# Optimization experiments

Hardware: AMD Instinct MI355X
Metric: run time of the kernel (lower is better)

## Reference

```python
import jax, jax.numpy as jnp
import numpy as np

T = 4096        # tokens
HC = 4          # hc_mult
HID = 4096      # hidden_size
MAX_IT = 20     # max_sk_it (nested: MAX_IT*MAX_IT inner iterations)
EPS = 1e-12


def setup_inputs() -> dict:
    key = jax.random.key(0)
    k1, k2, k3, k4 = jax.random.split(key, 4)
    out_dim = 2 * HC + HC * HC  # 24
    x = jax.random.normal(k1, (T, HC, HID), dtype=jnp.float32)
    weight = jax.random.normal(k2, (HC * HID, out_dim), dtype=jnp.float32) * 0.02
    bias = jax.random.normal(k3, (out_dim,), dtype=jnp.float32) * 0.02
    alpha = 1.0 + 0.1 * jax.random.normal(k4, (3,), dtype=jnp.float32)
    return {"x": x, "weight": weight, "bias": bias, "alpha": alpha}


def reference(x, weight, bias, alpha):
    t, hc, hid = x.shape
    xf = x.reshape(t, hc * hid)
    # RMSNorm scale absorbed into weight; only 1/rms applied explicitly
    r_inv = jax.lax.rsqrt(jnp.mean(xf * xf, axis=-1, keepdims=True))  # [t,1]
    h = xf.astype(jnp.float32) @ weight  # [t, 2*hc + hc*hc]
    h_pre = h[:, :hc]
    h_post = h[:, hc:2 * hc]
    h_res = h[:, 2 * hc:]
    h_pre = jax.nn.sigmoid(r_inv * alpha[0] * h_pre + bias[:hc])
    h_post = 2.0 * jax.nn.sigmoid(r_inv * alpha[1] * h_post + bias[hc:2 * hc])
    h_res_exp = jnp.exp((r_inv * alpha[2] * h_res + bias[2 * hc:]).reshape(t, hc, hc))

    # Sinkhorn-Knopp: original runs max_it outer x max_it inner identical updates
    u0 = jnp.ones((t, hc), jnp.float32)
    v0 = jnp.ones((t, hc), jnp.float32)

    def step(carry, _):
        u, v = carry
        uv = jnp.einsum('tij,tj->ti', h_res_exp, v)
        u = 1.0 / (uv + EPS)
        vu = jnp.einsum('tij,ti->tj', h_res_exp, u)
        v = 1.0 / (vu + EPS)
        return (u, v), None

    (u, v), _ = jax.lax.scan(step, (u0, v0), None, length=MAX_IT * MAX_IT)
    h_res_out = u[:, :, None] * h_res_exp * v[:, None, :]  # [t,hc,hc]
    return h_pre, h_post, h_res_out
```

## Files before the change

kernel.cpp:

```cpp
#include <hip/hip_runtime.h>
#include <hip/hip_bf16.h>


#define TROWS 4096
#define KDIM  16384
#define NOUT  24
#define RG    128
#define KC    32
#define KPER  (KDIM / KC)
#define TILEK 64
#define NTILE (KPER / TILEK)
#define XSTR  (RG + 1)

__device__ __forceinline__ float fast_rcp(float x)   { return __builtin_amdgcn_rcpf(x); }
__device__ __forceinline__ float fast_rsqrt(float x) { return __builtin_amdgcn_rsqf(x); }

__global__ __launch_bounds__(256) void gemv_part(const float* __restrict__ x,
                                                 const float* __restrict__ w,
                                                 float* __restrict__ hacc) {
    __shared__ float xT[TILEK * XSTR];
    __shared__ float wt[TILEK * NOUT];

    const int bid  = blockIdx.x;
    const int rb   = bid & 31;
    const int kc   = bid >> 5;
    const int rg0  = rb * RG;
    const int k0   = kc * KPER;

    const int t    = threadIdx.x;
    const int wv   = t >> 6;
    const int lane = t & 63;

    const int srow = t >> 4;
    const int sf4  = t & 15;
    const int kk   = sf4 * 4;

    float accA[NOUT + 1], accB[NOUT + 1];
#pragma unroll
    for (int j = 0; j <= NOUT; ++j) { accA[j] = 0.0f; accB[j] = 0.0f; }

    const float* xg = x + (size_t)rg0 * KDIM + k0;

    float4 px[8];
    float4 pw0, pw1;
    {
#pragma unroll
        for (int s = 0; s < 8; ++s)
            px[s] = *(const float4*)(xg + (size_t)(srow + 16 * s) * KDIM + kk);
        const float4* wg4 = (const float4*)(w + (size_t)k0 * NOUT);
        pw0 = wg4[t];
        pw1 = (t < 128) ? wg4[256 + t] : pw0;
    }

#pragma unroll 1
    for (int tile = 0; tile < NTILE; ++tile) {
        __syncthreads();
#pragma unroll
        for (int s = 0; s < 8; ++s) {
            const int row = srow + 16 * s;
            xT[(kk + 0) * XSTR + row] = px[s].x;
            xT[(kk + 1) * XSTR + row] = px[s].y;
            xT[(kk + 2) * XSTR + row] = px[s].z;
            xT[(kk + 3) * XSTR + row] = px[s].w;
        }
        ((float4*)wt)[t] = pw0;
        if (t < 128) ((float4*)wt)[256 + t] = pw1;
        __syncthreads();

        const int tn = (tile + 1 < NTILE) ? tile + 1 : tile;
        const int ktn = tn * TILEK;
#pragma unroll
        for (int s = 0; s < 8; ++s)
            px[s] = *(const float4*)(xg + (size_t)(srow + 16 * s) * KDIM + ktn + kk);
        {
            const float4* wg4 = (const float4*)(w + (size_t)(k0 + ktn) * NOUT);
            pw0 = wg4[t];
            pw1 = (t < 128) ? wg4[256 + t] : pw0;
        }

        const float* xk = xT + (wv * 16) * XSTR;
        const float* wk = wt + (wv * 16) * NOUT;
#pragma unroll
        for (int u = 0; u < 16; ++u) {
            const float xa = xk[u * XSTR + lane];
            const float xb = xk[u * XSTR + 64 + lane];
            const float4* wr = (const float4*)(wk + u * NOUT);
            float wbuf[24];
            *(float4*)(wbuf +  0) = wr[0];
            *(float4*)(wbuf +  4) = wr[1];
            *(float4*)(wbuf +  8) = wr[2];
            *(float4*)(wbuf + 12) = wr[3];
            *(float4*)(wbuf + 16) = wr[4];
            *(float4*)(wbuf + 20) = wr[5];
            accA[NOUT] = fmaf(xa, xa, accA[NOUT]);
            accB[NOUT] = fmaf(xb, xb, accB[NOUT]);
#pragma unroll
            for (int j = 0; j < NOUT; ++j) {
                accA[j] = fmaf(wbuf[j], xa, accA[j]);
                accB[j] = fmaf(wbuf[j], xb, accB[j]);
            }
        }
    }

#pragma unroll
    for (int j = 0; j <= NOUT; ++j) {
        atomicAdd(hacc + (size_t)j * TROWS + rg0 + lane,      accA[j]);
        atomicAdd(hacc + (size_t)j * TROWS + rg0 + 64 + lane, accB[j]);
    }
}

__global__ __launch_bounds__(64) void sinkhorn_epilogue(const float* __restrict__ hacc,
                                                        const float* __restrict__ bias,
                                                        const float* __restrict__ alpha,
                                                        float* __restrict__ out) {
    const int row = blockIdx.x * 64 + threadIdx.x;

    float h[25];
#pragma unroll
    for (int j = 0; j < 25; ++j) h[j] = hacc[(size_t)j * TROWS + row];

    const float r_inv = fast_rsqrt(h[24] * (1.0f / (float)KDIM));
    const float a0 = alpha[0], a1 = alpha[1], a2 = alpha[2];

#pragma unroll
    for (int i = 0; i < 4; ++i) {
        const float zpre = fmaf(r_inv * a0, h[i], bias[i]);
        out[(size_t)row * 4 + i] = fast_rcp(1.0f + __expf(-zpre));
        const float zpo = fmaf(r_inv * a1, h[4 + i], bias[4 + i]);
        out[(size_t)16384 + (size_t)row * 4 + i] = 2.0f * fast_rcp(1.0f + __expf(-zpo));
    }

    float E[16];
#pragma unroll
    for (int t = 0; t < 16; ++t)
        E[t] = __expf(fmaf(r_inv * a2, h[8 + t], bias[8 + t]));

    float u0 = 1.0f, u1 = 1.0f, u2 = 1.0f, u3 = 1.0f;
    float v0 = 1.0f, v1 = 1.0f, v2 = 1.0f, v3 = 1.0f;

#pragma unroll 1
    for (int it = 0; it < 400; ++it) {
        float s0 = fmaf(E[0],  v0, fmaf(E[1],  v1, fmaf(E[2],  v2, E[3]  * v3)));
        float s1 = fmaf(E[4],  v0, fmaf(E[5],  v1, fmaf(E[6],  v2, E[7]  * v3)));
        float s2 = fmaf(E[8],  v0, fmaf(E[9],  v1, fmaf(E[10], v2, E[11] * v3)));
        float s3 = fmaf(E[12], v0, fmaf(E[13], v1, fmaf(E[14], v2, E[15] * v3)));
        u0 = fast_rcp(s0 + 1e-12f);
        u1 = fast_rcp(s1 + 1e-12f);
        u2 = fast_rcp(s2 + 1e-12f);
        u3 = fast_rcp(s3 + 1e-12f);
        float t0 = fmaf(E[0], u0, fmaf(E[4], u1, fmaf(E[8],  u2, E[12] * u3)));
        float t1 = fmaf(E[1], u0, fmaf(E[5], u1, fmaf(E[9],  u2, E[13] * u3)));
        float t2 = fmaf(E[2], u0, fmaf(E[6], u1, fmaf(E[10], u2, E[14] * u3)));
        float t3 = fmaf(E[3], u0, fmaf(E[7], u1, fmaf(E[11], u2, E[15] * u3)));
        v0 = fast_rcp(t0 + 1e-12f);
        v1 = fast_rcp(t1 + 1e-12f);
        v2 = fast_rcp(t2 + 1e-12f);
        v3 = fast_rcp(t3 + 1e-12f);
    }

    const size_t ob = 32768 + (size_t)row * 16;
    out[ob + 0]  = u0 * E[0]  * v0;
    out[ob + 1]  = u0 * E[1]  * v1;
    out[ob + 2]  = u0 * E[2]  * v2;
    out[ob + 3]  = u0 * E[3]  * v3;
    out[ob + 4]  = u1 * E[4]  * v0;
    out[ob + 5]  = u1 * E[5]  * v1;
    out[ob + 6]  = u1 * E[6]  * v2;
    out[ob + 7]  = u1 * E[7]  * v3;
    out[ob + 8]  = u2 * E[8]  * v0;
    out[ob + 9]  = u2 * E[9]  * v1;
    out[ob + 10] = u2 * E[10] * v2;
    out[ob + 11] = u2 * E[11] * v3;
    out[ob + 12] = u3 * E[12] * v0;
    out[ob + 13] = u3 * E[13] * v1;
    out[ob + 14] = u3 * E[14] * v2;
    out[ob + 15] = u3 * E[15] * v3;
}

extern "C" void kernel_launch(void* const* d_in, const int* in_sizes, int n_in,
                              void* d_out, int out_size, void* d_ws, size_t ws_size,
                              hipStream_t stream) {
    const float* x     = (const float*)d_in[0];
    const float* w     = (const float*)d_in[1];
    const float* bias  = (const float*)d_in[2];
    const float* alpha = (const float*)d_in[3];
    float* out  = (float*)d_out;
    float* hacc = (float*)d_ws;

    hipMemsetAsync(hacc, 0, (size_t)(NOUT + 1) * TROWS * sizeof(float), stream);
    gemv_part<<<dim3(32 * KC), dim3(256), 0, stream>>>(x, w, hacc);
    sinkhorn_epilogue<<<dim3(TROWS / 64), dim3(64), 0, stream>>>(hacc, bias, alpha, out);
}
```

Before: 445.8 us.

## Enlarge GEMV row tile to 256 rows with 4 accumulators per thread

Doubles the rows per block to 256 and halves the K tile to 32, so each thread now accumulates four rows and each weight value loaded from LDS is reused four times instead of two. The x tile is stored row-major with padding instead of transposed, which makes the LDS writes float4-wide. The grid shrinks to 512 blocks and launch bounds request 2 blocks per CU. The trade-off is about 100 accumulator registers per thread and fewer blocks to hide memory latency on this memory-bound GEMV.

```diff
diff --git a/kernel.cpp b/kernel.cpp
--- a/kernel.cpp
+++ b/kernel.cpp
@@ -5,25 +5,25 @@
 #define TROWS 4096
 #define KDIM  16384
 #define NOUT  24
-#define RG    128
+#define RG    256
 #define KC    32
 #define KPER  (KDIM / KC)
-#define TILEK 64
+#define TILEK 32
 #define NTILE (KPER / TILEK)
-#define XSTR  (RG + 1)
+#define XSTR  (TILEK + 1)
 
 __device__ __forceinline__ float fast_rcp(float x)   { return __builtin_amdgcn_rcpf(x); }
 __device__ __forceinline__ float fast_rsqrt(float x) { return __builtin_amdgcn_rsqf(x); }
 
-__global__ __launch_bounds__(256) void gemv_part(const float* __restrict__ x,
-                                                 const float* __restrict__ w,
-                                                 float* __restrict__ hacc) {
-    __shared__ float xT[TILEK * XSTR];
+__global__ __launch_bounds__(256, 2) void gemv_part(const float* __restrict__ x,
+                                                    const float* __restrict__ w,
+                                                    float* __restrict__ hacc) {
+    __shared__ float xs[RG * XSTR];
     __shared__ float wt[TILEK * NOUT];
 
     const int bid  = blockIdx.x;
-    const int rb   = bid & 31;
-    const int kc   = bid >> 5;
+    const int rb   = bid & 15;
+    const int kc   = bid >> 4;
     const int rg0  = rb * RG;
     const int k0   = kc * KPER;
 
@@ -31,60 +31,56 @@
     const int wv   = t >> 6;
     const int lane = t & 63;
 
-    const int srow = t >> 4;
-    const int sf4  = t & 15;
+    const int srow = t >> 3;
+    const int sf4  = t & 7;
     const int kk   = sf4 * 4;
 
-    float accA[NOUT + 1], accB[NOUT + 1];
+    float acc[4][NOUT + 1];
 #pragma unroll
-    for (int j = 0; j <= NOUT; ++j) { accA[j] = 0.0f; accB[j] = 0.0f; }
+    for (int m = 0; m < 4; ++m)
+#pragma unroll
+        for (int j = 0; j <= NOUT; ++j) acc[m][j] = 0.0f;
 
     const float* xg = x + (size_t)rg0 * KDIM + k0;
 
     float4 px[8];
-    float4 pw0, pw1;
+    float4 pw;
     {
 #pragma unroll
         for (int s = 0; s < 8; ++s)
-            px[s] = *(const float4*)(xg + (size_t)(srow + 16 * s) * KDIM + kk);
+            px[s] = *(const float4*)(xg + (size_t)(32 * s + srow) * KDIM + kk);
         const float4* wg4 = (const float4*)(w + (size_t)k0 * NOUT);
-        pw0 = wg4[t];
-        pw1 = (t < 128) ? wg4[256 + t] : pw0;
+        pw = (t < 192) ? wg4[t] : make_float4(0.f, 0.f, 0.f, 0.f);
     }
 
 #pragma unroll 1
     for (int tile = 0; tile < NTILE; ++tile) {
         __syncthreads();
 #pragma unroll
-        for (int s = 0; s < 8; ++s) {
-            const int row = srow + 16 * s;
-            xT[(kk + 0) * XSTR + row] = px[s].x;
-            xT[(kk + 1) * XSTR + row] = px[s].y;
-            xT[(kk + 2) * XSTR + row] = px[s].z;
-            xT[(kk + 3) * XSTR + row] = px[s].w;
-        }
-        ((float4*)wt)[t] = pw0;
-        if (t < 128) ((float4*)wt)[256 + t] = pw1;
+        for (int s = 0; s < 8; ++s)
+            *(float4*)(xs + (32 * s + srow) * XSTR + kk) = px[s];
+        if (t < 192) ((float4*)wt)[t] = pw;
         __syncthreads();
 
-        const int tn = (tile + 1 < NTILE) ? tile + 1 : tile;
+        const int tn  = (tile + 1 < NTILE) ? tile + 1 : tile;
         const int ktn = tn * TILEK;
 #pragma unroll
         for (int s = 0; s < 8; ++s)
-            px[s] = *(const float4*)(xg + (size_t)(srow + 16 * s) * KDIM + ktn + kk);
+            px[s] = *(const float4*)(xg + (size_t)(32 * s + srow) * KDIM + ktn + kk);
         {
             const float4* wg4 = (const float4*)(w + (size_t)(k0 + ktn) * NOUT);
-            pw0 = wg4[t];
-            pw1 = (t < 128) ? wg4[256 + t] : pw0;
+            pw = (t < 192) ? wg4[t] : pw;
         }
 
-        const float* xk = xT + (wv * 16) * XSTR;
-        const float* wk = wt + (wv * 16) * NOUT;
 #pragma unroll
-        for (int u = 0; u < 16; ++u) {
-            const float xa = xk[u * XSTR + lane];
-            const float xb = xk[u * XSTR + 64 + lane];
-            const float4* wr = (const float4*)(wk + u * NOUT);
+        for (int u = 0; u < 8; ++u) {
+            const int kl = wv * 8 + u;
+            const float* xr = xs + kl;
+            const float x0 = xr[(lane      ) * XSTR];
+            const float x1 = xr[(lane +  64) * XSTR];
+            const float x2 = xr[(lane + 128) * XSTR];
+            const float x3 = xr[(lane + 192) * XSTR];
+            const float4* wr = (const float4*)(wt + kl * NOUT);
             float wbuf[24];
             *(float4*)(wbuf +  0) = wr[0];
             *(float4*)(wbuf +  4) = wr[1];
@@ -92,21 +88,25 @@
             *(float4*)(wbuf + 12) = wr[3];
             *(float4*)(wbuf + 16) = wr[4];
             *(float4*)(wbuf + 20) = wr[5];
-            accA[NOUT] = fmaf(xa, xa, accA[NOUT]);
-            accB[NOUT] = fmaf(xb, xb, accB[NOUT]);
+            acc[0][NOUT] = fmaf(x0, x0, acc[0][NOUT]);
+            acc[1][NOUT] = fmaf(x1, x1, acc[1][NOUT]);
+            acc[2][NOUT] = fmaf(x2, x2, acc[2][NOUT]);
+            acc[3][NOUT] = fmaf(x3, x3, acc[3][NOUT]);
 #pragma unroll
             for (int j = 0; j < NOUT; ++j) {
-                accA[j] = fmaf(wbuf[j], xa, accA[j]);
-                accB[j] = fmaf(wbuf[j], xb, accB[j]);
+                acc[0][j] = fmaf(wbuf[j], x0, acc[0][j]);
+                acc[1][j] = fmaf(wbuf[j], x1, acc[1][j]);
+                acc[2][j] = fmaf(wbuf[j], x2, acc[2][j]);
+                acc[3][j] = fmaf(wbuf[j], x3, acc[3][j]);
             }
         }
     }
 
 #pragma unroll
-    for (int j = 0; j <= NOUT; ++j) {
-        atomicAdd(hacc + (size_t)j * TROWS + rg0 + lane,      accA[j]);
-        atomicAdd(hacc + (size_t)j * TROWS + rg0 + 64 + lane, accB[j]);
-    }
+    for (int m = 0; m < 4; ++m)
+#pragma unroll
+        for (int j = 0; j <= NOUT; ++j)
+            atomicAdd(hacc + (size_t)j * TROWS + rg0 + 64 * m + lane, acc[m][j]);
 }
 
 __global__ __launch_bounds__(64) void sinkhorn_epilogue(const float* __restrict__ hacc,
@@ -188,6 +188,6 @@
     float* hacc = (float*)d_ws;
 
     hipMemsetAsync(hacc, 0, (size_t)(NOUT + 1) * TROWS * sizeof(float), stream);
-    gemv_part<<<dim3(32 * KC), dim3(256), 0, stream>>>(x, w, hacc);
+    gemv_part<<<dim3(16 * KC), dim3(256), 0, stream>>>(x, w, hacc);
     sinkhorn_epilogue<<<dim3(TROWS / 64), dim3(64), 0, stream>>>(hacc, bias, alpha, out);
 }
```

Result: slower. 499.9 us (+12.2%).
